# Kernel optimization log

Measured on AMD Instinct MI355X. Metric: run time of the kernel, lower is better.

The kernel has to match this reference:

```python
import jax, jax.numpy as jnp
import numpy as np

N = 1048576   # points
C = 50000     # clusters
F1, F2, FO = 128, 64, 64

def _lin(k, out_d, in_d):
    w = jax.random.normal(k, (out_d, in_d), jnp.float32) * (1.0 / np.sqrt(in_d))
    return w

def setup_inputs() -> dict:
    key = jax.random.key(0)
    ks = jax.random.split(key, 13)
    points = jax.random.normal(ks[0], (N, 3), jnp.float32)
    inv_feats = jax.random.normal(ks[1], (N, 4), jnp.float32)
    cluster = jax.random.randint(ks[2], (N,), 0, C, dtype=jnp.int32)
    return {
        "points": points, "inv_feats": inv_feats, "cluster": cluster,
        "W1": _lin(ks[3], F2, 4),       "b1": jnp.zeros((F2,), jnp.float32),
        "W2": _lin(ks[4], F1, F2),      "b2": jnp.zeros((F1,), jnp.float32),
        "W3": _lin(ks[5], F2, F1),      "b3": jnp.zeros((F2,), jnp.float32),
        "W4": _lin(ks[6], FO, F2),      "b4": jnp.zeros((FO,), jnp.float32),
        "W5": _lin(ks[7], 3, FO + 3),   "b5": jnp.zeros((3,), jnp.float32),
    }

def reference(points, inv_feats, cluster, W1, b1, W2, b2, W3, b3, W4, b4, W5, b5):
    relu = jax.nn.relu
    fc1 = relu(inv_feats @ W1.T + b1)                 # [N, F2]
    fc2 = relu(fc1 @ W2.T + b2)                       # [N, F1]
    # global_max_pool over clusters; fc2 >= 0 so clamping empty segments (-inf) to 0 is safe
    mx = jax.ops.segment_max(fc2, cluster, num_segments=C)
    mx = jnp.maximum(mx, 0.0)                         # [C, F1]
    fc3 = relu(mx @ W3.T + b3)                        # [C, F2]
    fc4 = relu(fc3 @ W4.T + b4)                       # [C, FO]
    repeated = fc4[cluster]                           # gather [N, FO]
    concat = jnp.concatenate([points, repeated], axis=-1)  # [N, FO+3]
    fc5 = relu(concat @ W5.T + b5)                    # [N, 3]
    sums = jax.ops.segment_sum(fc5, cluster, num_segments=C)
    cnt = jax.ops.segment_sum(jnp.ones((fc5.shape[0], 1), fc5.dtype), cluster, num_segments=C)
    angles = jax.nn.sigmoid(sums / jnp.maximum(cnt, 1.0))  # [C, 3]
    return (fc4, angles)
```

## Files before the change

### kernel.cpp

```cpp
#include <hip/hip_runtime.h>

#define N_PTS 1048576
#define NC 50000
#define SCAN_B 196

typedef int   i32x4  __attribute__((ext_vector_type(4)));
typedef float f32x4v __attribute__((ext_vector_type(4)));

__device__ __forceinline__ unsigned short bf16rne(float f) {
    unsigned u = __float_as_uint(f);
    u = (u + 0x7fffu + ((u >> 16) & 1u)) >> 16;
    return (unsigned short)u;
}
__device__ __forceinline__ f32x4v mfma16(i32x4 a, i32x4 b, f32x4v c) {
    asm("v_mfma_f32_16x16x32_bf16 %0, %1, %2, %0" : "+v"(c) : "v"(a), "v"(b));
    return c;
}
__device__ __forceinline__ int cvtpk(float lo, float hi) {
    int r;
    asm("v_cvt_pk_bf16_f32 %0, %1, %2" : "=v"(r) : "v"(lo), "v"(hi));
    return r;
}

#define DPPSHR(D, X) __builtin_amdgcn_update_dpp(0, (X), 0x110 | (D), 0xf, 0xf, true)
#define DPPSHL1(X)   __builtin_amdgcn_update_dpp(0, (X), 0x101, 0xf, 0xf, true)

__global__ __launch_bounds__(256) void k_prep(
    const float* __restrict__ W2, const float* __restrict__ W3,
    const float* __restrict__ W4,
    unsigned short* __restrict__ W2bf, unsigned short* __restrict__ W3bf,
    unsigned short* __restrict__ W4bf)
{
    int i = blockIdx.x * 256 + threadIdx.x;
    if (i < 8192)       W2bf[i]         = bf16rne(W2[i]);
    else if (i < 16384) W3bf[i - 8192]  = bf16rne(W3[i - 8192]);
    else                W4bf[i - 16384] = bf16rne(W4[i - 16384]);
}

__global__ __launch_bounds__(256) void k_hist(
    const int* __restrict__ cluster, int* __restrict__ counts)
{
    int i = blockIdx.x * 256 + threadIdx.x;
    atomicAdd(counts + cluster[i], 1);
}

__device__ __forceinline__ int block_excl_scan256(int v, int* lsum, int tid) {
    const int lane = tid & 63, wv = tid >> 6;
    int x = v, u;
    u = __shfl_up(x, 1, 64);  if (lane >= 1)  x += u;
    u = __shfl_up(x, 2, 64);  if (lane >= 2)  x += u;
    u = __shfl_up(x, 4, 64);  if (lane >= 4)  x += u;
    u = __shfl_up(x, 8, 64);  if (lane >= 8)  x += u;
    u = __shfl_up(x, 16, 64); if (lane >= 16) x += u;
    u = __shfl_up(x, 32, 64); if (lane >= 32) x += u;
    if (lane == 63) lsum[wv] = x;
    __syncthreads();
    int woff = 0;
    if (wv > 0) woff += lsum[0];
    if (wv > 1) woff += lsum[1];
    if (wv > 2) woff += lsum[2];
    return woff + x - v;
}

__global__ __launch_bounds__(256) void k_scanA(
    const int* __restrict__ counts, int* __restrict__ partial)
{
    __shared__ int lsum[4];
    int i = blockIdx.x * 256 + threadIdx.x;
    int v = (i < NC) ? counts[i] : 0;
    int e = block_excl_scan256(v, lsum, threadIdx.x);
    if (threadIdx.x == 255) partial[blockIdx.x] = e + v;
}

__global__ __launch_bounds__(256) void k_scanB(int* __restrict__ partial)
{
    __shared__ int lsum[4];
    int tid = threadIdx.x;
    int v = (tid < SCAN_B) ? partial[tid] : 0;
    int e = block_excl_scan256(v, lsum, tid);
    __syncthreads();
    if (tid < SCAN_B) partial[tid] = e;
}

__global__ __launch_bounds__(256) void k_scanC(
    const int* __restrict__ counts, const int* __restrict__ partial,
    int* __restrict__ cursor)
{
    __shared__ int lsum[4];
    int i = blockIdx.x * 256 + threadIdx.x;
    int v = (i < NC) ? counts[i] : 0;
    int e = block_excl_scan256(v, lsum, threadIdx.x);
    if (i < NC) cursor[i] = partial[blockIdx.x] + e;
}

__global__ __launch_bounds__(256) void k_scatter(
    const int* __restrict__ cluster, int* __restrict__ cursor,
    int* __restrict__ perm, int* __restrict__ pclus)
{
    int i = blockIdx.x * 256 + threadIdx.x;
    int c = cluster[i];
    int pos = atomicAdd(cursor + c, 1);
    perm[pos] = i;
    pclus[pos] = c;
}

__global__ __launch_bounds__(256, 4) void k_points_mfma(
    const float* __restrict__ inv_feats,
    const int* __restrict__ perm, const int* __restrict__ pclus,
    const float* __restrict__ W1, const float* __restrict__ b1,
    const unsigned short* __restrict__ W2bf, const float* __restrict__ b2,
    float* __restrict__ mx)
{
    const int tid  = threadIdx.x;
    const int wv   = tid >> 6;
    const int l    = tid & 63;
    const int base = (blockIdx.x * 4 + wv) * 32;
    const int m16 = l & 15;
    const int g4  = (l >> 4) * 4;
    const int k8  = (l >> 4) * 8;

    const int pA = perm[base + m16];
    const int pB = perm[base + 16 + m16];
    const float4 xA = *(const float4*)(inv_feats + (size_t)pA * 4);
    const float4 xB = *(const float4*)(inv_feats + (size_t)pB * 4);

#define FC1(K, X, Q) float Q; { \
    const float4 w = *(const float4*)(W1 + (size_t)(K) * 4); \
    float a = b1[K]; \
    a = fmaf(w.x, X.x, a); a = fmaf(w.y, X.y, a); \
    a = fmaf(w.z, X.z, a); a = fmaf(w.w, X.w, a); \
    Q = fmaxf(a, 0.f); }
#define PKD(BF, D, K, X) { FC1((K), X, qe) FC1((K) + 1, X, qo) BF[D] = cvtpk(qe, qo); }

    i32x4 b00, b01, b10, b11;
    PKD(b00, 0, k8 + 0, xA) PKD(b00, 1, k8 + 2, xA)
    PKD(b00, 2, k8 + 4, xA) PKD(b00, 3, k8 + 6, xA)
    PKD(b01, 0, 32 + k8 + 0, xA) PKD(b01, 1, 32 + k8 + 2, xA)
    PKD(b01, 2, 32 + k8 + 4, xA) PKD(b01, 3, 32 + k8 + 6, xA)
    PKD(b10, 0, k8 + 0, xB) PKD(b10, 1, k8 + 2, xB)
    PKD(b10, 2, k8 + 4, xB) PKD(b10, 3, k8 + 6, xB)
    PKD(b11, 0, 32 + k8 + 0, xB) PKD(b11, 1, 32 + k8 + 2, xB)
    PKD(b11, 2, 32 + k8 + 4, xB) PKD(b11, 3, 32 + k8 + 6, xB)
#undef PKD
#undef FC1

    const int cp0 = pclus[base + m16] + 1;
    const int cp1 = pclus[base + 16 + m16] + 1;
    const bool e0a = (DPPSHR(1, cp0) == cp0);
    const bool e0b = (DPPSHR(2, cp0) == cp0);
    const bool e0c = (DPPSHR(4, cp0) == cp0);
    const bool e0d = (DPPSHR(8, cp0) == cp0);
    const bool tl0 = (DPPSHL1(cp0) != cp0);
    const bool e1a = (DPPSHR(1, cp1) == cp1);
    const bool e1b = (DPPSHR(2, cp1) == cp1);
    const bool e1c = (DPPSHR(4, cp1) == cp1);
    const bool e1d = (DPPSHR(8, cp1) == cp1);
    const bool tl1 = (DPPSHL1(cp1) != cp1);
    int* mrow0 = (int*)mx + (size_t)(cp0 - 1) * 128;
    int* mrow1 = (int*)mx + (size_t)(cp1 - 1) * 128;

#define LDA(MB, KK) (*(const i32x4*)(W2bf + (size_t)(kcc + (MB)*16 + m16) * 64 + (KK)*32 + k8))

#define SC4(V, EA, EB, EC, ED) { float _u; \
    _u = __int_as_float(DPPSHR(1, __float_as_int(V))); if (EA) V = fmaxf(V, _u); \
    _u = __int_as_float(DPPSHR(2, __float_as_int(V))); if (EB) V = fmaxf(V, _u); \
    _u = __int_as_float(DPPSHR(4, __float_as_int(V))); if (EC) V = fmaxf(V, _u); \
    _u = __int_as_float(DPPSHR(8, __float_as_int(V))); if (ED) V = fmaxf(V, _u); }

#define EMIT(ACC, MB, EA, EB, EC, ED, TL, MROW) { \
    const float4 bb = *(const float4*)(b2 + kcc + (MB)*16 + g4); \
    float v0 = fmaxf(ACC[0] + bb.x, 0.f); \
    float v1 = fmaxf(ACC[1] + bb.y, 0.f); \
    float v2 = fmaxf(ACC[2] + bb.z, 0.f); \
    float v3 = fmaxf(ACC[3] + bb.w, 0.f); \
    SC4(v0, EA, EB, EC, ED) SC4(v1, EA, EB, EC, ED) \
    SC4(v2, EA, EB, EC, ED) SC4(v3, EA, EB, EC, ED) \
    if (TL) { \
        if (v0 > 0.f) atomicMax(MROW + kcc + (MB)*16 + g4 + 0, __float_as_int(v0)); \
        if (v1 > 0.f) atomicMax(MROW + kcc + (MB)*16 + g4 + 1, __float_as_int(v1)); \
        if (v2 > 0.f) atomicMax(MROW + kcc + (MB)*16 + g4 + 2, __float_as_int(v2)); \
        if (v3 > 0.f) atomicMax(MROW + kcc + (MB)*16 + g4 + 3, __float_as_int(v3)); } }

#define PASS(KC) { \
    const int kcc = (KC) * 64; \
    const i32x4 a00 = LDA(0,0), a01 = LDA(0,1), a10 = LDA(1,0), a11 = LDA(1,1); \
    const i32x4 a20 = LDA(2,0), a21 = LDA(2,1), a30 = LDA(3,0), a31 = LDA(3,1); \
    f32x4v c00 = {0.f,0.f,0.f,0.f}, c01 = {0.f,0.f,0.f,0.f}; \
    f32x4v c10 = {0.f,0.f,0.f,0.f}, c11 = {0.f,0.f,0.f,0.f}; \
    f32x4v c20 = {0.f,0.f,0.f,0.f}, c21 = {0.f,0.f,0.f,0.f}; \
    f32x4v c30 = {0.f,0.f,0.f,0.f}, c31 = {0.f,0.f,0.f,0.f}; \
    c00 = mfma16(a00, b00, c00); c00 = mfma16(a01, b01, c00); \
    c10 = mfma16(a10, b00, c10); c10 = mfma16(a11, b01, c10); \
    c20 = mfma16(a20, b00, c20); c20 = mfma16(a21, b01, c20); \
    c30 = mfma16(a30, b00, c30); c30 = mfma16(a31, b01, c30); \
    c01 = mfma16(a00, b10, c01); c01 = mfma16(a01, b11, c01); \
    c11 = mfma16(a10, b10, c11); c11 = mfma16(a11, b11, c11); \
    c21 = mfma16(a20, b10, c21); c21 = mfma16(a21, b11, c21); \
    c31 = mfma16(a30, b10, c31); c31 = mfma16(a31, b11, c31); \
    EMIT(c00, 0, e0a, e0b, e0c, e0d, tl0, mrow0) \
    EMIT(c10, 1, e0a, e0b, e0c, e0d, tl0, mrow0) \
    EMIT(c20, 2, e0a, e0b, e0c, e0d, tl0, mrow0) \
    EMIT(c30, 3, e0a, e0b, e0c, e0d, tl0, mrow0) \
    EMIT(c01, 0, e1a, e1b, e1c, e1d, tl1, mrow1) \
    EMIT(c11, 1, e1a, e1b, e1c, e1d, tl1, mrow1) \
    EMIT(c21, 2, e1a, e1b, e1c, e1d, tl1, mrow1) \
    EMIT(c31, 3, e1a, e1b, e1c, e1d, tl1, mrow1) }

    PASS(0)
    PASS(1)
#undef PASS
#undef EMIT
#undef SC4
#undef LDA
}

__global__ __launch_bounds__(256, 4) void k_cluster_mfma(
    const float* __restrict__ mx,
    const unsigned short* __restrict__ W3bf, const float* __restrict__ b3,
    const unsigned short* __restrict__ W4bf, const float* __restrict__ b4,
    float* __restrict__ fc4out)
{
    __shared__ __align__(16) unsigned short f3[4][32 * 64];
    const int tid = threadIdx.x;
    const int wv  = tid >> 6;
    const int l   = tid & 63;
    const int m16 = l & 15;
    const int g4  = (l >> 4) * 4;
    const int k8  = (l >> 4) * 8;
    const int cbase = (blockIdx.x * 4 + wv) * 32;
    const int cA = cbase + m16;
    const int cB = cbase + 16 + m16;
    const size_t rA = (size_t)min(cA, NC - 1) * 128;
    const size_t rB = (size_t)min(cB, NC - 1) * 128;
    unsigned short* f3w = &f3[wv][0];
    const int swA = (m16 & 7) << 3;
    const int swB = swA;

    f32x4v d00 = {0,0,0,0}, d01 = {0,0,0,0}, d02 = {0,0,0,0}, d03 = {0,0,0,0};
    f32x4v d10 = {0,0,0,0}, d11 = {0,0,0,0}, d12 = {0,0,0,0}, d13 = {0,0,0,0};

#define LD3(MB, KK) (*(const i32x4*)(W3bf + (size_t)((MB)*16 + m16) * 128 + (KK)*32 + k8))
#define FC3STEP(KK) { \
    const float4 vA0 = *(const float4*)(mx + rA + (KK)*32 + k8); \
    const float4 vA1 = *(const float4*)(mx + rA + (KK)*32 + k8 + 4); \
    const float4 vB0 = *(const float4*)(mx + rB + (KK)*32 + k8); \
    const float4 vB1 = *(const float4*)(mx + rB + (KK)*32 + k8 + 4); \
    i32x4 bA = { cvtpk(vA0.x, vA0.y), cvtpk(vA0.z, vA0.w), \
                 cvtpk(vA1.x, vA1.y), cvtpk(vA1.z, vA1.w) }; \
    i32x4 bB = { cvtpk(vB0.x, vB0.y), cvtpk(vB0.z, vB0.w), \
                 cvtpk(vB1.x, vB1.y), cvtpk(vB1.z, vB1.w) }; \
    const i32x4 a0 = LD3(0, KK), a1 = LD3(1, KK), a2 = LD3(2, KK), a3 = LD3(3, KK); \
    d00 = mfma16(a0, bA, d00); d01 = mfma16(a1, bA, d01); \
    d02 = mfma16(a2, bA, d02); d03 = mfma16(a3, bA, d03); \
    d10 = mfma16(a0, bB, d10); d11 = mfma16(a1, bB, d11); \
    d12 = mfma16(a2, bB, d12); d13 = mfma16(a3, bB, d13); }
    FC3STEP(0) FC3STEP(1) FC3STEP(2) FC3STEP(3)
#undef FC3STEP
#undef LD3

#define ST3(DD, MB, CL, SW) { \
    const float4 bb = *(const float4*)(b3 + (MB)*16 + g4); \
    float v0 = fmaxf(DD[0] + bb.x, 0.f); \
    float v1 = fmaxf(DD[1] + bb.y, 0.f); \
    float v2 = fmaxf(DD[2] + bb.z, 0.f); \
    float v3 = fmaxf(DD[3] + bb.w, 0.f); \
    int2 pk = { cvtpk(v0, v1), cvtpk(v2, v3) }; \
    *(int2*)(f3w + (CL)*64 + ((((MB)*16 + g4)) ^ (SW))) = pk; }
    ST3(d00, 0, m16, swA) ST3(d01, 1, m16, swA) ST3(d02, 2, m16, swA) ST3(d03, 3, m16, swA)
    ST3(d10, 0, 16 + m16, swB) ST3(d11, 1, 16 + m16, swB) ST3(d12, 2, 16 + m16, swB) ST3(d13, 3, 16 + m16, swB)
#undef ST3

    f32x4v e00 = {0,0,0,0}, e01 = {0,0,0,0}, e02 = {0,0,0,0}, e03 = {0,0,0,0};
    f32x4v e10 = {0,0,0,0}, e11 = {0,0,0,0}, e12 = {0,0,0,0}, e13 = {0,0,0,0};
#define LD4(MB, KK) (*(const i32x4*)(W4bf + (size_t)((MB)*16 + m16) * 64 + (KK)*32 + k8))
#define FC4STEP(KK) { \
    const i32x4 bA4 = *(const i32x4*)(f3w + m16*64 + (((KK)*32 + k8) ^ swA)); \
    const i32x4 bB4 = *(const i32x4*)(f3w + (16 + m16)*64 + (((KK)*32 + k8) ^ swB)); \
    const i32x4 a0 = LD4(0, KK), a1 = LD4(1, KK), a2 = LD4(2, KK), a3 = LD4(3, KK); \
    e00 = mfma16(a0, bA4, e00); e01 = mfma16(a1, bA4, e01); \
    e02 = mfma16(a2, bA4, e02); e03 = mfma16(a3, bA4, e03); \
    e10 = mfma16(a0, bB4, e10); e11 = mfma16(a1, bB4, e11); \
    e12 = mfma16(a2, bB4, e12); e13 = mfma16(a3, bB4, e13); }
    FC4STEP(0) FC4STEP(1)
#undef FC4STEP
#undef LD4

#define WR(EE, MB, CL) if ((CL) < NC) { \
    const float4 bb = *(const float4*)(b4 + (MB)*16 + g4); \
    float4 o; \
    o.x = fmaxf(EE[0] + bb.x, 0.f); \
    o.y = fmaxf(EE[1] + bb.y, 0.f); \
    o.z = fmaxf(EE[2] + bb.z, 0.f); \
    o.w = fmaxf(EE[3] + bb.w, 0.f); \
    *(float4*)(fc4out + (size_t)(CL)*64 + (MB)*16 + g4) = o; }
    WR(e00, 0, cA) WR(e01, 1, cA) WR(e02, 2, cA) WR(e03, 3, cA)
    WR(e10, 0, cB) WR(e11, 1, cB) WR(e12, 2, cB) WR(e13, 3, cB)
#undef WR
}

__global__ __launch_bounds__(256) void k_fc5_sorted(
    const float* __restrict__ points,
    const int* __restrict__ perm, const int* __restrict__ pclus,
    const float* __restrict__ fc4, const float* __restrict__ W5,
    const float* __restrict__ b5, float* __restrict__ sums)
{
    const int t = blockIdx.x * 256 + threadIdx.x;
    const int p = perm[t];
    const int c = pclus[t];
    const float p0 = points[(size_t)p * 3 + 0];
    const float p1 = points[(size_t)p * 3 + 1];
    const float p2 = points[(size_t)p * 3 + 2];
    const float* f4 = fc4 + (size_t)c * 64;

    float a0 = b5[0];
    a0 = fmaf(W5[0], p0, a0); a0 = fmaf(W5[1], p1, a0); a0 = fmaf(W5[2], p2, a0);
    float a1 = b5[1];
    a1 = fmaf(W5[67], p0, a1); a1 = fmaf(W5[68], p1, a1); a1 = fmaf(W5[69], p2, a1);
    float a2 = b5[2];
    a2 = fmaf(W5[134], p0, a2); a2 = fmaf(W5[135], p1, a2); a2 = fmaf(W5[136], p2, a2);

#pragma unroll
    for (int j = 0; j < 64; j += 4) {
        float4 v = *(const float4*)(f4 + j);
        a0 = fmaf(W5[3 + j + 0], v.x, a0);
        a0 = fmaf(W5[3 + j + 1], v.y, a0);
        a0 = fmaf(W5[3 + j + 2], v.z, a0);
        a0 = fmaf(W5[3 + j + 3], v.w, a0);
        a1 = fmaf(W5[70 + j + 0], v.x, a1);
        a1 = fmaf(W5[70 + j + 1], v.y, a1);
        a1 = fmaf(W5[70 + j + 2], v.z, a1);
        a1 = fmaf(W5[70 + j + 3], v.w, a1);
        a2 = fmaf(W5[137 + j + 0], v.x, a2);
        a2 = fmaf(W5[137 + j + 1], v.y, a2);
        a2 = fmaf(W5[137 + j + 2], v.z, a2);
        a2 = fmaf(W5[137 + j + 3], v.w, a2);
    }
    a0 = fmaxf(a0, 0.f);
    a1 = fmaxf(a1, 0.f);
    a2 = fmaxf(a2, 0.f);

    const int lane = threadIdx.x & 63;
    const int cu1  = __shfl_up(c, 1, 64);
    const int cu2  = __shfl_up(c, 2, 64);
    const int cu4  = __shfl_up(c, 4, 64);
    const int cu8  = __shfl_up(c, 8, 64);
    const int cu16 = __shfl_up(c, 16, 64);
    const int cu32 = __shfl_up(c, 32, 64);
    const int cdn  = __shfl_down(c, 1, 64);
    const bool eq0 = (lane >= 1)  && (cu1  == c);
    const bool eq1 = (lane >= 2)  && (cu2  == c);
    const bool eq2 = (lane >= 4)  && (cu4  == c);
    const bool eq3 = (lane >= 8)  && (cu8  == c);
    const bool eq4 = (lane >= 16) && (cu16 == c);
    const bool eq5 = (lane >= 32) && (cu32 == c);
    const bool tail = (lane == 63) || (cdn != c);

    float u0, u1, u2;
    u0 = __shfl_up(a0, 1, 64);  u1 = __shfl_up(a1, 1, 64);  u2 = __shfl_up(a2, 1, 64);
    if (eq0) { a0 += u0; a1 += u1; a2 += u2; }
    u0 = __shfl_up(a0, 2, 64);  u1 = __shfl_up(a1, 2, 64);  u2 = __shfl_up(a2, 2, 64);
    if (eq1) { a0 += u0; a1 += u1; a2 += u2; }
    u0 = __shfl_up(a0, 4, 64);  u1 = __shfl_up(a1, 4, 64);  u2 = __shfl_up(a2, 4, 64);
    if (eq2) { a0 += u0; a1 += u1; a2 += u2; }
    u0 = __shfl_up(a0, 8, 64);  u1 = __shfl_up(a1, 8, 64);  u2 = __shfl_up(a2, 8, 64);
    if (eq3) { a0 += u0; a1 += u1; a2 += u2; }
    u0 = __shfl_up(a0, 16, 64); u1 = __shfl_up(a1, 16, 64); u2 = __shfl_up(a2, 16, 64);
    if (eq4) { a0 += u0; a1 += u1; a2 += u2; }
    u0 = __shfl_up(a0, 32, 64); u1 = __shfl_up(a1, 32, 64); u2 = __shfl_up(a2, 32, 64);
    if (eq5) { a0 += u0; a1 += u1; a2 += u2; }

    if (tail) {
        float* srow = sums + (size_t)c * 3;
        atomicAdd(srow + 0, a0);
        atomicAdd(srow + 1, a1);
        atomicAdd(srow + 2, a2);
    }
}

__global__ __launch_bounds__(256) void k_angles(
    const float* __restrict__ sums, const int* __restrict__ counts,
    float* __restrict__ angout)
{
    int c = blockIdx.x * 256 + threadIdx.x;
    if (c >= NC) return;
    const float cnt = fmaxf((float)counts[c], 1.f);
#pragma unroll
    for (int r = 0; r < 3; ++r) {
        float s = sums[(size_t)c * 3 + r] / cnt;
        angout[(size_t)c * 3 + r] = 1.f / (1.f + expf(-s));
    }
}

extern "C" void kernel_launch(void* const* d_in, const int* in_sizes, int n_in,
                              void* d_out, int out_size, void* d_ws, size_t ws_size,
                              hipStream_t stream) {
    const float* points  = (const float*)d_in[0];
    const float* inv     = (const float*)d_in[1];
    const int*   cluster = (const int*)d_in[2];
    const float* W1 = (const float*)d_in[3];
    const float* b1 = (const float*)d_in[4];
    const float* W2 = (const float*)d_in[5];
    const float* b2 = (const float*)d_in[6];
    const float* W3 = (const float*)d_in[7];
    const float* b3 = (const float*)d_in[8];
    const float* W4 = (const float*)d_in[9];
    const float* b4 = (const float*)d_in[10];
    const float* W5 = (const float*)d_in[11];
    const float* b5 = (const float*)d_in[12];

    float* out    = (float*)d_out;
    float* fc4out = out;
    float* angout = out + (size_t)NC * 64;

    int*   counts = (int*)d_ws;
    float* sums   = (float*)(counts + NC);
    float* mx     = sums + (size_t)NC * 3;
    int*   cursor = (int*)(mx + (size_t)NC * 128);
    int*   perm   = cursor + NC;
    int*   pclus  = perm + N_PTS;
    unsigned short* W2bf = (unsigned short*)(pclus + N_PTS);
    unsigned short* W3bf = W2bf + 8192;
    unsigned short* W4bf = W3bf + 8192;
    int*   partial = (int*)(W4bf + 4096);

    hipMemsetAsync(d_ws, 0, (size_t)(NC + NC * 3 + NC * 128) * sizeof(float), stream);

    k_prep         <<<80, 256, 0, stream>>>(W2, W3, W4, W2bf, W3bf, W4bf);
    k_hist         <<<N_PTS / 256, 256, 0, stream>>>(cluster, counts);
    k_scanA        <<<SCAN_B, 256, 0, stream>>>(counts, partial);
    k_scanB        <<<1, 256, 0, stream>>>(partial);
    k_scanC        <<<SCAN_B, 256, 0, stream>>>(counts, partial, cursor);
    k_scatter      <<<N_PTS / 256, 256, 0, stream>>>(cluster, cursor, perm, pclus);
    k_points_mfma  <<<N_PTS / 128, 256, 0, stream>>>(inv, perm, pclus, W1, b1, W2bf, b2, mx);
    k_cluster_mfma <<<(NC + 127) / 128, 256, 0, stream>>>(mx, W3bf, b3, W4bf, b4, fc4out);
    k_fc5_sorted   <<<N_PTS / 256, 256, 0, stream>>>(points, perm, pclus, fc4out, W5, b5, sums);
    k_angles       <<<(NC + 255) / 256, 256, 0, stream>>>(sums, counts, angout);
}
```

Before: 327.4 us.

## Precompute per-cluster fc5 partial products and pack perm/cluster into int2

Adds a per-cluster kernel that computes the fc4 part of fc5 (W5[:,3:]·fc4 + b5) once per cluster. The per-point fc5 kernel then reads one float4 per point instead of re-reading 64 floats of fc4 and running 192 FMAs. The permutation and cluster-id arrays are also merged into one int2 array, so scatter writes and later kernels load both with a single access. The cost is one extra small kernel launch and a small per-cluster scratch buffer.

```diff
diff --git a/kernel.cpp b/kernel.cpp
--- a/kernel.cpp
+++ b/kernel.cpp
@@ -95,18 +95,18 @@
 
 __global__ __launch_bounds__(256) void k_scatter(
     const int* __restrict__ cluster, int* __restrict__ cursor,
-    int* __restrict__ perm, int* __restrict__ pclus)
+    int2* __restrict__ pp)
 {
     int i = blockIdx.x * 256 + threadIdx.x;
     int c = cluster[i];
     int pos = atomicAdd(cursor + c, 1);
-    perm[pos] = i;
-    pclus[pos] = c;
+    int2 v = { i, c };
+    pp[pos] = v;
 }
 
 __global__ __launch_bounds__(256, 4) void k_points_mfma(
     const float* __restrict__ inv_feats,
-    const int* __restrict__ perm, const int* __restrict__ pclus,
+    const int2* __restrict__ pp,
     const float* __restrict__ W1, const float* __restrict__ b1,
     const unsigned short* __restrict__ W2bf, const float* __restrict__ b2,
     float* __restrict__ mx)
@@ -119,10 +119,10 @@
     const int g4  = (l >> 4) * 4;
     const int k8  = (l >> 4) * 8;
 
-    const int pA = perm[base + m16];
-    const int pB = perm[base + 16 + m16];
-    const float4 xA = *(const float4*)(inv_feats + (size_t)pA * 4);
-    const float4 xB = *(const float4*)(inv_feats + (size_t)pB * 4);
+    const int2 ppA = pp[base + m16];
+    const int2 ppB = pp[base + 16 + m16];
+    const float4 xA = *(const float4*)(inv_feats + (size_t)ppA.x * 4);
+    const float4 xB = *(const float4*)(inv_feats + (size_t)ppB.x * 4);
 
 #define FC1(K, X, Q) float Q; { \
     const float4 w = *(const float4*)(W1 + (size_t)(K) * 4); \
@@ -144,8 +144,8 @@
 #undef PKD
 #undef FC1
 
-    const int cp0 = pclus[base + m16] + 1;
-    const int cp1 = pclus[base + 16 + m16] + 1;
+    const int cp0 = ppA.y + 1;
+    const int cp1 = ppB.y + 1;
     const bool e0a = (DPPSHR(1, cp0) == cp0);
     const bool e0b = (DPPSHR(2, cp0) == cp0);
     const bool e0c = (DPPSHR(4, cp0) == cp0);
@@ -298,43 +298,47 @@
 #undef WR
 }
 
+__global__ __launch_bounds__(256) void k_g(
+    const float* __restrict__ fc4, const float* __restrict__ W5,
+    const float* __restrict__ b5, float* __restrict__ g)
+{
+    int c = blockIdx.x * 256 + threadIdx.x;
+    if (c >= NC) return;
+    const float* f4 = fc4 + (size_t)c * 64;
+    float a0 = b5[0], a1 = b5[1], a2 = b5[2];
+#pragma unroll
+    for (int j = 0; j < 64; j += 4) {
+        float4 v = *(const float4*)(f4 + j);
+        a0 = fmaf(W5[3 + j], v.x, a0);  a0 = fmaf(W5[4 + j], v.y, a0);
+        a0 = fmaf(W5[5 + j], v.z, a0);  a0 = fmaf(W5[6 + j], v.w, a0);
+        a1 = fmaf(W5[70 + j], v.x, a1); a1 = fmaf(W5[71 + j], v.y, a1);
+        a1 = fmaf(W5[72 + j], v.z, a1); a1 = fmaf(W5[73 + j], v.w, a1);
+        a2 = fmaf(W5[137 + j], v.x, a2); a2 = fmaf(W5[138 + j], v.y, a2);
+        a2 = fmaf(W5[139 + j], v.z, a2); a2 = fmaf(W5[140 + j], v.w, a2);
+    }
+    float4 o = { a0, a1, a2, 0.f };
+    *(float4*)(g + (size_t)c * 4) = o;
+}
+
 __global__ __launch_bounds__(256) void k_fc5_sorted(
     const float* __restrict__ points,
-    const int* __restrict__ perm, const int* __restrict__ pclus,
-    const float* __restrict__ fc4, const float* __restrict__ W5,
-    const float* __restrict__ b5, float* __restrict__ sums)
+    const int2* __restrict__ pp,
+    const float* __restrict__ g, const float* __restrict__ W5,
+    float* __restrict__ sums)
 {
     const int t = blockIdx.x * 256 + threadIdx.x;
-    const int p = perm[t];
-    const int c = pclus[t];
+    const int2 pc = pp[t];
+    const int p = pc.x;
+    const int c = pc.y;
     const float p0 = points[(size_t)p * 3 + 0];
     const float p1 = points[(size_t)p * 3 + 1];
     const float p2 = points[(size_t)p * 3 + 2];
-    const float* f4 = fc4 + (size_t)c * 64;
-
-    float a0 = b5[0];
-    a0 = fmaf(W5[0], p0, a0); a0 = fmaf(W5[1], p1, a0); a0 = fmaf(W5[2], p2, a0);
-    float a1 = b5[1];
-    a1 = fmaf(W5[67], p0, a1); a1 = fmaf(W5[68], p1, a1); a1 = fmaf(W5[69], p2, a1);
-    float a2 = b5[2];
+    const float4 gg = *(const float4*)(g + (size_t)c * 4);
+
+    float a0 = gg.x, a1 = gg.y, a2 = gg.z;
+    a0 = fmaf(W5[0], p0, a0);   a0 = fmaf(W5[1], p1, a0);   a0 = fmaf(W5[2], p2, a0);
+    a1 = fmaf(W5[67], p0, a1);  a1 = fmaf(W5[68], p1, a1);  a1 = fmaf(W5[69], p2, a1);
     a2 = fmaf(W5[134], p0, a2); a2 = fmaf(W5[135], p1, a2); a2 = fmaf(W5[136], p2, a2);
-
-#pragma unroll
-    for (int j = 0; j < 64; j += 4) {
-        float4 v = *(const float4*)(f4 + j);
-        a0 = fmaf(W5[3 + j + 0], v.x, a0);
-        a0 = fmaf(W5[3 + j + 1], v.y, a0);
-        a0 = fmaf(W5[3 + j + 2], v.z, a0);
-        a0 = fmaf(W5[3 + j + 3], v.w, a0);
-        a1 = fmaf(W5[70 + j + 0], v.x, a1);
-        a1 = fmaf(W5[70 + j + 1], v.y, a1);
-        a1 = fmaf(W5[70 + j + 2], v.z, a1);
-        a1 = fmaf(W5[70 + j + 3], v.w, a1);
-        a2 = fmaf(W5[137 + j + 0], v.x, a2);
-        a2 = fmaf(W5[137 + j + 1], v.y, a2);
-        a2 = fmaf(W5[137 + j + 2], v.z, a2);
-        a2 = fmaf(W5[137 + j + 3], v.w, a2);
-    }
     a0 = fmaxf(a0, 0.f);
     a1 = fmaxf(a1, 0.f);
     a2 = fmaxf(a2, 0.f);
@@ -416,12 +420,12 @@
     float* sums   = (float*)(counts + NC);
     float* mx     = sums + (size_t)NC * 3;
     int*   cursor = (int*)(mx + (size_t)NC * 128);
-    int*   perm   = cursor + NC;
-    int*   pclus  = perm + N_PTS;
-    unsigned short* W2bf = (unsigned short*)(pclus + N_PTS);
+    int2*  pp     = (int2*)(cursor + NC);
+    unsigned short* W2bf = (unsigned short*)(pp + N_PTS);
     unsigned short* W3bf = W2bf + 8192;
     unsigned short* W4bf = W3bf + 8192;
     int*   partial = (int*)(W4bf + 4096);
+    float* g       = (float*)(partial + 256);
 
     hipMemsetAsync(d_ws, 0, (size_t)(NC + NC * 3 + NC * 128) * sizeof(float), stream);
 
@@ -430,9 +434,10 @@
     k_scanA        <<<SCAN_B, 256, 0, stream>>>(counts, partial);
     k_scanB        <<<1, 256, 0, stream>>>(partial);
     k_scanC        <<<SCAN_B, 256, 0, stream>>>(counts, partial, cursor);
-    k_scatter      <<<N_PTS / 256, 256, 0, stream>>>(cluster, cursor, perm, pclus);
-    k_points_mfma  <<<N_PTS / 128, 256, 0, stream>>>(inv, perm, pclus, W1, b1, W2bf, b2, mx);
+    k_scatter      <<<N_PTS / 256, 256, 0, stream>>>(cluster, cursor, pp);
+    k_points_mfma  <<<N_PTS / 128, 256, 0, stream>>>(inv, pp, W1, b1, W2bf, b2, mx);
     k_cluster_mfma <<<(NC + 127) / 128, 256, 0, stream>>>(mx, W3bf, b3, W4bf, b4, fc4out);
-    k_fc5_sorted   <<<N_PTS / 256, 256, 0, stream>>>(points, perm, pclus, fc4out, W5, b5, sums);
+    k_g            <<<(NC + 255) / 256, 256, 0, stream>>>(fc4out, W5, b5, g);
+    k_fc5_sorted   <<<N_PTS / 256, 256, 0, stream>>>(points, pp, g, W5, sums);
     k_angles       <<<(NC + 255) / 256, 256, 0, stream>>>(sums, counts, angout);
 }
```

Result: slower. 336.6 us (+2.8%).
